# Performance work log

Hardware: AMD Instinct MI355X
Metric: run time of the kernel (lower is better)

Reference implementation:

```python
import jax, jax.numpy as jnp
import numpy as np

D, H = 1024, 2048
N_STEPS = 2
T0, T1 = 0.0, 1.0


def setup_inputs() -> dict:
    key = jax.random.key(0)
    ks = jax.random.split(key, 5)
    s_in = 1.0 / np.sqrt(D)
    s_h = 1.0 / np.sqrt(H)
    return {
        "x0": jax.random.normal(ks[0], (D,), jnp.float32),
        "W1": jax.random.normal(ks[1], (D, H), jnp.float32) * s_in,
        "b1": jnp.zeros((H,), jnp.float32),
        "wt": jax.random.normal(ks[2], (H,), jnp.float32) * 0.1,
        "W2": jax.random.normal(ks[3], (H, H), jnp.float32) * s_h,
        "b2": jnp.zeros((H,), jnp.float32),
        "W3": jax.random.normal(ks[4], (H, D), jnp.float32) * s_h,
        "b3": jnp.zeros((D,), jnp.float32),
    }


def reference(x0, W1, b1, wt, W2, b2, W3, b3):
    dtype = x0.dtype

    def velocity(t, x):
        # 3-layer tanh MLP velocity field with additive time embedding
        h1 = jnp.tanh(x @ W1 + b1 + t * wt)
        h2 = jnp.tanh(h1 @ W2 + b2)
        return h2 @ W3 + b3

    def vel_and_div(t, x):
        # Mirror of _compute_velocity_and_divergence: linearize + vmap(jvp)
        # over identity to get the full Jacobian, then take its trace.
        v, jvp_fun = jax.linearize(lambda z: velocity(t, z), x)
        cols = jax.vmap(jvp_fun)(jnp.eye(D, dtype=dtype))  # [D, D]
        return v, jnp.trace(cols)

    def aug_dyn(t, x):
        v, div = vel_and_div(t, x)
        return v, -div  # (dx/dt, dlogq/dt)

    # Standard-normal base distribution log_prob at x0
    log2pi = jnp.log(jnp.asarray(2.0 * np.pi, dtype=dtype))
    logq0 = -0.5 * jnp.sum(x0 * x0) - 0.5 * D * log2pi

    dt = jnp.asarray((T1 - T0) / N_STEPS, dtype=dtype)

    def rk4_step(carry, i):
        x, logq = carry
        t = T0 + i * dt
        v1, dl1 = aug_dyn(t, x)
        v2, dl2 = aug_dyn(t + 0.5 * dt, x + 0.5 * dt * v1)
        v3, dl3 = aug_dyn(t + 0.5 * dt, x + 0.5 * dt * v2)
        v4, dl4 = aug_dyn(t + dt, x + dt * v3)
        x_new = x + (dt / 6.0) * (v1 + 2.0 * v2 + 2.0 * v3 + v4)
        logq_new = logq + (dt / 6.0) * (dl1 + 2.0 * dl2 + 2.0 * dl3 + dl4)
        return (x_new, logq_new), None

    (x1, logq1), _ = jax.lax.scan(
        rk4_step, (x0, logq0), jnp.arange(N_STEPS, dtype=dtype)
    )
    # concat [x1 (D,), logq1 ()] -> (D+1,) for a single output array
    return jnp.concatenate([x1, logq1[None]])
```

## Files before the change

kernel.cpp:

```cpp
#include <hip/hip_runtime.h>
#include <math.h>

#define DD 1024
#define HH 2048
#define NCB 256

typedef float f32x4 __attribute__((ext_vector_type(4)));
typedef short short8 __attribute__((ext_vector_type(8)));

__device__ __forceinline__ float b2f(unsigned short u) {
    return __uint_as_float(((unsigned int)u) << 16);
}
__device__ __forceinline__ unsigned short f2b(float f) {
    unsigned int x = __float_as_uint(f);
    unsigned int r = (x + 0x7FFFu + ((x >> 16) & 1u)) >> 16;
    return (unsigned short)r;
}
__device__ __forceinline__ float ald(const float* p) {
    return __hip_atomic_load(p, __ATOMIC_RELAXED, __HIP_MEMORY_SCOPE_AGENT);
}
__device__ __forceinline__ void ast(float* p, float v) {
    __hip_atomic_store(p, v, __ATOMIC_RELAXED, __HIP_MEMORY_SCOPE_AGENT);
}

__global__ __launch_bounds__(256) void k_tr(const float* __restrict__ W1,
                                            const float* __restrict__ W2,
                                            const float* __restrict__ W3,
                                            unsigned short* __restrict__ W1T,
                                            unsigned short* __restrict__ W2T,
                                            unsigned short* __restrict__ W3T,
                                            unsigned short* __restrict__ W3b,
                                            unsigned* __restrict__ sync) {
    __shared__ float tile[64][65];
    const int b = blockIdx.x, t = threadIdx.x;
    if (b == 0) {
        #pragma unroll
        for (int q = 0; q < 18; ++q) {
            int i = t + q * 256;
            if (i < 4368) sync[i] = 0u;
        }
    }
    const float* in; unsigned short* out; int R, C, bx, by;
    bool isW3 = false;
    if (b < 512)       { int bb = b;        in = W1; out = W1T; R = DD; C = HH; bx = bb & 31; by = bb >> 5; }
    else if (b < 1536) { int bb = b - 512;  in = W2; out = W2T; R = HH; C = HH; bx = bb & 31; by = bb >> 5; }
    else               { int bb = b - 1536; in = W3; out = W3T; R = HH; C = DD; bx = bb & 15; by = bb >> 4; isW3 = true; }
    const int c0 = bx * 64, r0 = by * 64;
    const int cc = t & 63, rb = t >> 6;
    #pragma unroll
    for (int p = 0; p < 16; ++p) {
        int rr = p * 4 + rb;
        float v = in[(size_t)(r0 + rr) * C + c0 + cc];
        tile[rr][cc] = v;
        if (isW3) W3b[(size_t)(r0 + rr) * DD + c0 + cc] = f2b(v);
    }
    __syncthreads();
    #pragma unroll
    for (int p = 0; p < 16; ++p) {
        int rr = p * 4 + rb;
        out[(size_t)(c0 + rr) * R + r0 + cc] = f2b(tile[cc][rr]);
    }
}

__global__ __launch_bounds__(256) void k_gemmP(const unsigned short* __restrict__ W1T,
                                               const unsigned short* __restrict__ W3b,
                                               const float* __restrict__ W2,
                                               const float* __restrict__ b3,
                                               const float* __restrict__ x0,
                                               unsigned short* __restrict__ Mb,
                                               unsigned short* __restrict__ Pb,
                                               float* __restrict__ c1,
                                               float* __restrict__ A1g) {
    __shared__ unsigned short At[128][40];
    __shared__ unsigned short Bt[128][40];
    const int b = blockIdx.x, t = threadIdx.x;
    const int m0 = (b & 15) * 128;
    const int k0 = (b >> 4) * 128;
    const int r = t & 127, half = t >> 7;
    const int wv = t >> 6, l = t & 63;
    const int wr = wv >> 1, wc = wv & 1;
    const int fr = l & 15, fg = l >> 4;
    const bool do_aux = ((b >> 4) == 0) && (t < 128);
    float c1acc = 0.f, a1acc = 0.f;

    f32x4 acc[4][4] = {};
    for (int i0 = 0; i0 < DD; i0 += 32) {
        {
            const float4* sa = (const float4*)(W1T + (size_t)(m0 + r) * DD + i0 + half * 16);
            const float4* sb = (const float4*)(W3b + (size_t)(k0 + r) * DD + i0 + half * 16);
            float4 a0 = sa[0], a1 = sa[1];
            float4 b0 = sb[0], b1 = sb[1];
            float4* da = (float4*)&At[r][half * 16];
            float4* db = (float4*)&Bt[r][half * 16];
            da[0] = a0; da[1] = a1;
            db[0] = b0; db[1] = b1;
        }
        __syncthreads();
        if (do_aux) {
            #pragma unroll
            for (int i = 0; i < 32; ++i) {
                float w1v = b2f(At[t][i]);
                c1acc += w1v * b3[i0 + i];
                a1acc += w1v * x0[i0 + i];
            }
        }
        short8 af[4], bf[4];
        #pragma unroll
        for (int a = 0; a < 4; ++a)
            af[a] = *(const short8*)&At[wr * 64 + a * 16 + fr][fg * 8];
        #pragma unroll
        for (int bq = 0; bq < 4; ++bq)
            bf[bq] = *(const short8*)&Bt[wc * 64 + bq * 16 + fr][fg * 8];
        #pragma unroll
        for (int a = 0; a < 4; ++a)
            #pragma unroll
            for (int bq = 0; bq < 4; ++bq)
                acc[a][bq] = __builtin_amdgcn_mfma_f32_16x16x32_bf16(af[a], bf[bq], acc[a][bq], 0, 0, 0);
        __syncthreads();
    }
    if (do_aux) { c1[m0 + t] = c1acc; A1g[m0 + t] = a1acc; }
    #pragma unroll
    for (int a = 0; a < 4; ++a) {
        #pragma unroll
        for (int bq = 0; bq < 4; ++bq) {
            #pragma unroll
            for (int j = 0; j < 4; ++j) {
                int row = m0 + wr * 64 + a * 16 + fg * 4 + j;
                int col = k0 + wc * 64 + bq * 16 + fr;
                size_t idx = (size_t)row * HH + col;
                float m = acc[a][bq][j];
                Mb[idx] = f2b(m);
                Pb[idx] = f2b(m * W2[idx]);
            }
        }
    }
}

__device__ __forceinline__ void gbar(unsigned* sync, int b, unsigned g) {
    __syncthreads();
    if (threadIdx.x < 64) {
        if (threadIdx.x == 0) {
            asm volatile("s_waitcnt vmcnt(0)" ::: "memory");
            __hip_atomic_store(&sync[b << 4], g, __ATOMIC_RELAXED, __HIP_MEMORY_SCOPE_AGENT);
        }
        while (true) {
            bool ok = true;
            #pragma unroll
            for (int k = 0; k < 4; ++k) {
                unsigned f = __hip_atomic_load(&sync[(threadIdx.x + (k << 6)) << 4],
                                               __ATOMIC_RELAXED, __HIP_MEMORY_SCOPE_AGENT);
                ok &= (f >= g);
            }
            if (!__any((int)(!ok))) break;
            __builtin_amdgcn_s_sleep(1);
        }
    }
    __syncthreads();
}

__global__ __launch_bounds__(256, 1) void k_chain(
    const unsigned short* __restrict__ Mb,
    const unsigned short* __restrict__ Pb,
    const unsigned short* __restrict__ W2T,
    const unsigned short* __restrict__ W3T,
    const float* __restrict__ x0,
    const float* __restrict__ b1, const float* __restrict__ wt,
    const float* __restrict__ b2, const float* __restrict__ b3,
    const float* __restrict__ c1, const float* __restrict__ A1g,
    float* __restrict__ h1_g, float* __restrict__ h2_g, float* __restrict__ hacc_g,
    float* __restrict__ out,
    unsigned* __restrict__ sync) {
    __shared__ unsigned short Ms[8][2048];
    __shared__ unsigned short Ps[8][2048];
    __shared__ unsigned short Qs[8][2048];
    __shared__ float vecH[2048];
    __shared__ float vecW[2048];
    __shared__ float wred[4];
    const int t = threadIdx.x, b = blockIdx.x;
    const int wib = t >> 6, lane = t & 63;
    const int gw2 = (b << 3) + (wib << 1);
    const int jx = (b << 2) + wib;
    unsigned g = 0;

    {
        const unsigned short* mp = Mb + (size_t)gw2 * HH;
        const unsigned short* pp = Pb + (size_t)gw2 * HH;
        const unsigned short* qp = W2T + (size_t)gw2 * HH;
        #pragma unroll
        for (int rep = 0; rep < 4; ++rep) {
            const int idx = rep * 512 + lane * 8;
            *(short8*)&Ms[wib * 2][idx]     = *(const short8*)(mp + idx);
            *(short8*)&Ms[wib * 2 + 1][idx] = *(const short8*)(mp + HH + idx);
            *(short8*)&Ps[wib * 2][idx]     = *(const short8*)(pp + idx);
            *(short8*)&Ps[wib * 2 + 1][idx] = *(const short8*)(pp + HH + idx);
            *(short8*)&Qs[wib * 2][idx]     = *(const short8*)(qp + idx);
            *(short8*)&Qs[wib * 2 + 1][idx] = *(const short8*)(qp + HH + idx);
        }
    }

    const float bb1_0 = b1[gw2], bb1_1 = b1[gw2 + 1];
    const float wt_0 = wt[gw2], wt_1 = wt[gw2 + 1];
    const float bb2_0 = b2[gw2], bb2_1 = b2[gw2 + 1];
    const float c1_0 = c1[gw2], c1_1 = c1[gw2 + 1];

    float A1_0 = 0.f, A1_1 = 0.f;
    float u0 = 0.f, u1 = 0.f;
    float hc0 = 0.f, hc1 = 0.f;
    float wdiv = 0.f;

    float logq_r = 0.f;
    if (b == 0 && wib == 0) {
        float ssum = 0.f;
        #pragma unroll
        for (int q = 0; q < 16; ++q) { float xv = x0[lane + (q << 6)]; ssum += xv * xv; }
        #pragma unroll
        for (int o = 1; o < 64; o <<= 1) ssum += __shfl_xor(ssum, o, 64);
        logq_r = -0.5f * ssum - 0.5f * 1024.0f * 1.8378770664093453f;
    }

    for (int s = 0; s < 8; ++s) {
        const int ss = s & 3;
        const float tcur = (s >> 2) * 0.5f + ((ss == 0) ? 0.f : (ss == 3) ? 0.5f : 0.25f);

        if (s == 0) {
            A1_0 = A1g[gw2]; A1_1 = A1g[gw2 + 1];
            float h0 = tanhf(A1_0 + bb1_0 + tcur * wt_0);
            float h1v = tanhf(A1_1 + bb1_1 + tcur * wt_1);
            u0 = 1.f - h0 * h0; u1 = 1.f - h1v * h1v;
            if (lane == 0) { ast(h1_g + gw2, h0); ast(h1_g + gw2 + 1, h1v); }
        } else {
            #pragma unroll
            for (int q = 0; q < 8; ++q) {
                int i = t + (q << 8);
                float h2v = ald(h2_g + i);
                float sv = (ss == 0) ? ald(hacc_g + i) : h2v;
                vecH[i] = sv;
                vecW[i] = 1.f - h2v * h2v;
            }
            __syncthreads();
            float md0 = 0.f, md1 = 0.f, pd0 = 0.f, pd1 = 0.f;
            #pragma unroll
            for (int rep = 0; rep < 4; ++rep) {
                const int idx = rep * 512 + lane * 8;
                float4 hA = *(const float4*)(vecH + idx);
                float4 hB = *(const float4*)(vecH + idx + 4);
                float4 wA = *(const float4*)(vecW + idx);
                float4 wB = *(const float4*)(vecW + idx + 4);
                float hv[8] = {hA.x, hA.y, hA.z, hA.w, hB.x, hB.y, hB.z, hB.w};
                float wv[8] = {wA.x, wA.y, wA.z, wA.w, wB.x, wB.y, wB.z, wB.w};
                short8 m0v = *(const short8*)&Ms[wib * 2][idx];
                short8 m1v = *(const short8*)&Ms[wib * 2 + 1][idx];
                short8 p0v = *(const short8*)&Ps[wib * 2][idx];
                short8 p1v = *(const short8*)&Ps[wib * 2 + 1][idx];
                #pragma unroll
                for (int e = 0; e < 8; ++e) {
                    md0 += b2f((unsigned short)m0v[e]) * hv[e];
                    md1 += b2f((unsigned short)m1v[e]) * hv[e];
                    pd0 += b2f((unsigned short)p0v[e]) * wv[e];
                    pd1 += b2f((unsigned short)p1v[e]) * wv[e];
                }
            }
            #pragma unroll
            for (int o = 1; o < 64; o <<= 1) {
                md0 += __shfl_xor(md0, o, 64); md1 += __shfl_xor(md1, o, 64);
                pd0 += __shfl_xor(pd0, o, 64); pd1 += __shfl_xor(pd1, o, 64);
            }
            const int sp = (s - 1) & 3;
            const float cprev = (sp == 1 || sp == 2) ? (1.f / 6.f) : (1.f / 12.f);
            wdiv += cprev * (u0 * pd0 + u1 * pd1);
            float pre0, pre1;
            if (ss == 0) {
                A1_0 += md0 + 0.5f * c1_0; A1_1 += md1 + 0.5f * c1_1;
                pre0 = A1_0 + bb1_0 + tcur * wt_0; pre1 = A1_1 + bb1_1 + tcur * wt_1;
            } else {
                const float a = (ss == 3) ? 0.5f : 0.25f;
                pre0 = A1_0 + a * (md0 + c1_0) + bb1_0 + tcur * wt_0;
                pre1 = A1_1 + a * (md1 + c1_1) + bb1_1 + tcur * wt_1;
            }
            float h0 = tanhf(pre0), h1v = tanhf(pre1);
            u0 = 1.f - h0 * h0; u1 = 1.f - h1v * h1v;
            if (lane == 0) { ast(h1_g + gw2, h0); ast(h1_g + gw2 + 1, h1v); }
        }
        gbar(sync, b, ++g);

        #pragma unroll
        for (int q = 0; q < 8; ++q) {
            int i = t + (q << 8);
            vecH[i] = ald(h1_g + i);
        }
        __syncthreads();
        {
            float a0 = 0.f, a1 = 0.f;
            #pragma unroll
            for (int rep = 0; rep < 4; ++rep) {
                const int idx = rep * 512 + lane * 8;
                float4 hA = *(const float4*)(vecH + idx);
                float4 hB = *(const float4*)(vecH + idx + 4);
                float hv[8] = {hA.x, hA.y, hA.z, hA.w, hB.x, hB.y, hB.z, hB.w};
                short8 r0 = *(const short8*)&Qs[wib * 2][idx];
                short8 r1 = *(const short8*)&Qs[wib * 2 + 1][idx];
                #pragma unroll
                for (int e = 0; e < 8; ++e) {
                    a0 += b2f((unsigned short)r0[e]) * hv[e];
                    a1 += b2f((unsigned short)r1[e]) * hv[e];
                }
            }
            #pragma unroll
            for (int o = 1; o < 64; o <<= 1) {
                a0 += __shfl_xor(a0, o, 64); a1 += __shfl_xor(a1, o, 64);
            }
            float q0 = tanhf(a0 + bb2_0), q1 = tanhf(a1 + bb2_1);
            const float cs = (ss == 1 || ss == 2) ? (1.f / 6.f) : (1.f / 12.f);
            hc0 += cs * q0; hc1 += cs * q1;
            if (lane == 0) {
                ast(h2_g + gw2, q0); ast(h2_g + gw2 + 1, q1);
                if (ss == 3) { ast(hacc_g + gw2, hc0); ast(hacc_g + gw2 + 1, hc1); }
            }
        }
        gbar(sync, b, ++g);
    }

    {
        #pragma unroll
        for (int q = 0; q < 8; ++q) {
            int i = t + (q << 8);
            float h2v = ald(h2_g + i);
            vecH[i] = ald(hacc_g + i);
            vecW[i] = 1.f - h2v * h2v;
        }
        __syncthreads();
        float pd0 = 0.f, pd1 = 0.f, xo = 0.f;
        const unsigned short* Vr = W3T + (size_t)jx * HH;
        #pragma unroll
        for (int rep = 0; rep < 4; ++rep) {
            const int idx = rep * 512 + lane * 8;
            float4 cA = *(const float4*)(vecH + idx);
            float4 cB = *(const float4*)(vecH + idx + 4);
            float4 wA = *(const float4*)(vecW + idx);
            float4 wB = *(const float4*)(vecW + idx + 4);
            float cv[8] = {cA.x, cA.y, cA.z, cA.w, cB.x, cB.y, cB.z, cB.w};
            float wv[8] = {wA.x, wA.y, wA.z, wA.w, wB.x, wB.y, wB.z, wB.w};
            short8 p0v = *(const short8*)&Ps[wib * 2][idx];
            short8 p1v = *(const short8*)&Ps[wib * 2 + 1][idx];
            short8 vv = *(const short8*)(Vr + idx);
            #pragma unroll
            for (int e = 0; e < 8; ++e) {
                pd0 += b2f((unsigned short)p0v[e]) * wv[e];
                pd1 += b2f((unsigned short)p1v[e]) * wv[e];
                xo  += b2f((unsigned short)vv[e]) * cv[e];
            }
        }
        #pragma unroll
        for (int o = 1; o < 64; o <<= 1) {
            pd0 += __shfl_xor(pd0, o, 64); pd1 += __shfl_xor(pd1, o, 64);
            xo += __shfl_xor(xo, o, 64);
        }
        wdiv += (1.f / 12.f) * (u0 * pd0 + u1 * pd1);
        if (lane == 0) {
            out[jx] = x0[jx] + xo + b3[jx];
            wred[wib] = wdiv;
        }
    }
    __syncthreads();
    if (t == 0) {
        float dsum = wred[0] + wred[1] + wred[2] + wred[3];
        atomicAdd((float*)(sync + 4096 + (b & 15) * 16), dsum);
        asm volatile("s_waitcnt vmcnt(0)" ::: "memory");
        atomicAdd(sync + 4352, 1u);
    }
    if (b == 0 && wib == 0) {
        if (lane == 0) {
            while (__hip_atomic_load(sync + 4352, __ATOMIC_RELAXED, __HIP_MEMORY_SCOPE_AGENT) < NCB)
                __builtin_amdgcn_s_sleep(2);
        }
        float v = 0.f;
        if (lane < 16) {
            unsigned du = __hip_atomic_load(sync + 4096 + lane * 16,
                                            __ATOMIC_RELAXED, __HIP_MEMORY_SCOPE_AGENT);
            v = __uint_as_float(du);
        }
        #pragma unroll
        for (int o = 1; o < 64; o <<= 1) v += __shfl_xor(v, o, 64);
        if (lane == 0) out[DD] = logq_r - v;
    }
}

extern "C" void kernel_launch(void* const* d_in, const int* in_sizes, int n_in,
                              void* d_out, int out_size, void* d_ws, size_t ws_size,
                              hipStream_t stream) {
    const float* x0 = (const float*)d_in[0];
    const float* W1 = (const float*)d_in[1];
    const float* b1 = (const float*)d_in[2];
    const float* wt = (const float*)d_in[3];
    const float* W2 = (const float*)d_in[4];
    const float* b2 = (const float*)d_in[5];
    const float* W3 = (const float*)d_in[6];
    const float* b3 = (const float*)d_in[7];
    float* out = (float*)d_out;

    char* ws = (char*)d_ws;
    const size_t MB = 1024 * 1024;
    unsigned short* Pb  = (unsigned short*)(ws);
    unsigned short* W2T = (unsigned short*)(ws + 8 * MB);
    unsigned short* W3T = (unsigned short*)(ws + 16 * MB);
    unsigned short* Mb  = (unsigned short*)(ws + 20 * MB);
    unsigned short* W1T = (unsigned short*)(ws + 28 * MB);
    unsigned short* W3b = (unsigned short*)(ws + 32 * MB);
    float* fb = (float*)(ws + 36 * MB);
    float* c1      = fb;
    float* A1g     = fb + 2048;
    float* h1_g    = fb + 4096;
    float* h2_g    = fb + 6144;
    float* hacc_g  = fb + 8192;
    unsigned* sync = (unsigned*)(fb + 10240);

    k_tr<<<2048, 256, 0, stream>>>(W1, W2, W3, W1T, W2T, W3T, W3b, sync);
    k_gemmP<<<256, 256, 0, stream>>>(W1T, W3b, W2, b3, x0, Mb, Pb, c1, A1g);
    k_chain<<<NCB, 256, 0, stream>>>(Mb, Pb, W2T, W3T, x0, b1, wt, b2, b3, c1, A1g,
                                     h1_g, h2_g, hacc_g, out, sync);
}
```

Baseline: 164.5 us.

## Split global barrier to overlap shared-memory preloads, halve GEMM tile height

The precompute GEMM now uses 64x128 tiles across 512 blocks instead of 128x128 across 256, giving more parallelism on a GPU with many compute units. In the chain kernel the grid barrier is split into separate arrive and wait halves. The W2T and then the M/P matrix loads into shared memory are issued between arrive and wait, so they overlap with the barrier spin. The first stage (h1 and the h2 matvec at t=0) is peeled out of the loop to make this possible. The cost is more code, and the GEMM tiles get less reuse of the B tile.

```diff
diff --git a/kernel.cpp b/kernel.cpp
--- a/kernel.cpp
+++ b/kernel.cpp
@@ -71,28 +71,27 @@
                                                unsigned short* __restrict__ Pb,
                                                float* __restrict__ c1,
                                                float* __restrict__ A1g) {
-    __shared__ unsigned short At[128][40];
+    __shared__ unsigned short At[64][40];
     __shared__ unsigned short Bt[128][40];
     const int b = blockIdx.x, t = threadIdx.x;
-    const int m0 = (b & 15) * 128;
-    const int k0 = (b >> 4) * 128;
-    const int r = t & 127, half = t >> 7;
+    const int m0 = (b & 31) * 64;
+    const int k0 = (b >> 5) * 128;
     const int wv = t >> 6, l = t & 63;
-    const int wr = wv >> 1, wc = wv & 1;
     const int fr = l & 15, fg = l >> 4;
-    const bool do_aux = ((b >> 4) == 0) && (t < 128);
+    const int ra = t & 63, ha = t >> 6;
+    const int rb2 = t & 127, hb = t >> 7;
+    const bool do_aux = ((b >> 5) == 0) && (t < 64);
     float c1acc = 0.f, a1acc = 0.f;
 
-    f32x4 acc[4][4] = {};
+    f32x4 acc[4][2] = {};
     for (int i0 = 0; i0 < DD; i0 += 32) {
         {
-            const float4* sa = (const float4*)(W1T + (size_t)(m0 + r) * DD + i0 + half * 16);
-            const float4* sb = (const float4*)(W3b + (size_t)(k0 + r) * DD + i0 + half * 16);
-            float4 a0 = sa[0], a1 = sa[1];
+            const float4* sa = (const float4*)(W1T + (size_t)(m0 + ra) * DD + i0 + ha * 8);
+            float4 a0 = sa[0];
+            const float4* sb = (const float4*)(W3b + (size_t)(k0 + rb2) * DD + i0 + hb * 16);
             float4 b0 = sb[0], b1 = sb[1];
-            float4* da = (float4*)&At[r][half * 16];
-            float4* db = (float4*)&Bt[r][half * 16];
-            da[0] = a0; da[1] = a1;
+            *(float4*)&At[ra][ha * 8] = a0;
+            float4* db = (float4*)&Bt[rb2][hb * 16];
             db[0] = b0; db[1] = b1;
         }
         __syncthreads();
@@ -104,17 +103,17 @@
                 a1acc += w1v * x0[i0 + i];
             }
         }
-        short8 af[4], bf[4];
+        short8 af[4], bf[2];
         #pragma unroll
         for (int a = 0; a < 4; ++a)
-            af[a] = *(const short8*)&At[wr * 64 + a * 16 + fr][fg * 8];
-        #pragma unroll
-        for (int bq = 0; bq < 4; ++bq)
-            bf[bq] = *(const short8*)&Bt[wc * 64 + bq * 16 + fr][fg * 8];
+            af[a] = *(const short8*)&At[a * 16 + fr][fg * 8];
+        #pragma unroll
+        for (int bq = 0; bq < 2; ++bq)
+            bf[bq] = *(const short8*)&Bt[wv * 32 + bq * 16 + fr][fg * 8];
         #pragma unroll
         for (int a = 0; a < 4; ++a)
             #pragma unroll
-            for (int bq = 0; bq < 4; ++bq)
+            for (int bq = 0; bq < 2; ++bq)
                 acc[a][bq] = __builtin_amdgcn_mfma_f32_16x16x32_bf16(af[a], bf[bq], acc[a][bq], 0, 0, 0);
         __syncthreads();
     }
@@ -122,11 +121,11 @@
     #pragma unroll
     for (int a = 0; a < 4; ++a) {
         #pragma unroll
-        for (int bq = 0; bq < 4; ++bq) {
+        for (int bq = 0; bq < 2; ++bq) {
             #pragma unroll
             for (int j = 0; j < 4; ++j) {
-                int row = m0 + wr * 64 + a * 16 + fg * 4 + j;
-                int col = k0 + wc * 64 + bq * 16 + fr;
+                int row = m0 + a * 16 + fg * 4 + j;
+                int col = k0 + wv * 32 + bq * 16 + fr;
                 size_t idx = (size_t)row * HH + col;
                 float m = acc[a][bq][j];
                 Mb[idx] = f2b(m);
@@ -136,13 +135,15 @@
     }
 }
 
-__device__ __forceinline__ void gbar(unsigned* sync, int b, unsigned g) {
+__device__ __forceinline__ void garrive(unsigned* sync, int b, unsigned g) {
     __syncthreads();
+    if (threadIdx.x == 0) {
+        asm volatile("s_waitcnt vmcnt(0)" ::: "memory");
+        __hip_atomic_store(&sync[b << 4], g, __ATOMIC_RELAXED, __HIP_MEMORY_SCOPE_AGENT);
+    }
+}
+__device__ __forceinline__ void gwait(unsigned* sync, unsigned g) {
     if (threadIdx.x < 64) {
-        if (threadIdx.x == 0) {
-            asm volatile("s_waitcnt vmcnt(0)" ::: "memory");
-            __hip_atomic_store(&sync[b << 4], g, __ATOMIC_RELAXED, __HIP_MEMORY_SCOPE_AGENT);
-        }
         while (true) {
             bool ok = true;
             #pragma unroll
@@ -156,6 +157,10 @@
         }
     }
     __syncthreads();
+}
+__device__ __forceinline__ void gbar(unsigned* sync, int b, unsigned g) {
+    garrive(sync, b, g);
+    gwait(sync, g);
 }
 
 __global__ __launch_bounds__(256, 1) void k_chain(
@@ -182,21 +187,9 @@
     const int jx = (b << 2) + wib;
     unsigned g = 0;
 
-    {
-        const unsigned short* mp = Mb + (size_t)gw2 * HH;
-        const unsigned short* pp = Pb + (size_t)gw2 * HH;
-        const unsigned short* qp = W2T + (size_t)gw2 * HH;
-        #pragma unroll
-        for (int rep = 0; rep < 4; ++rep) {
-            const int idx = rep * 512 + lane * 8;
-            *(short8*)&Ms[wib * 2][idx]     = *(const short8*)(mp + idx);
-            *(short8*)&Ms[wib * 2 + 1][idx] = *(const short8*)(mp + HH + idx);
-            *(short8*)&Ps[wib * 2][idx]     = *(const short8*)(pp + idx);
-            *(short8*)&Ps[wib * 2 + 1][idx] = *(const short8*)(pp + HH + idx);
-            *(short8*)&Qs[wib * 2][idx]     = *(const short8*)(qp + idx);
-            *(short8*)&Qs[wib * 2 + 1][idx] = *(const short8*)(qp + HH + idx);
-        }
-    }
+    const unsigned short* mp = Mb + (size_t)gw2 * HH;
+    const unsigned short* pp = Pb + (size_t)gw2 * HH;
+    const unsigned short* qp = W2T + (size_t)gw2 * HH;
 
     const float bb1_0 = b1[gw2], bb1_1 = b1[gw2 + 1];
     const float wt_0 = wt[gw2], wt_1 = wt[gw2 + 1];
@@ -218,17 +211,70 @@
         logq_r = -0.5f * ssum - 0.5f * 1024.0f * 1.8378770664093453f;
     }
 
-    for (int s = 0; s < 8; ++s) {
+    {
+        A1_0 = A1g[gw2]; A1_1 = A1g[gw2 + 1];
+        float h0 = tanhf(A1_0 + bb1_0);
+        float h1v = tanhf(A1_1 + bb1_1);
+        u0 = 1.f - h0 * h0; u1 = 1.f - h1v * h1v;
+        if (lane == 0) { ast(h1_g + gw2, h0); ast(h1_g + gw2 + 1, h1v); }
+    }
+    garrive(sync, b, ++g);
+    #pragma unroll
+    for (int rep = 0; rep < 4; ++rep) {
+        const int idx = rep * 512 + lane * 8;
+        *(short8*)&Qs[wib * 2][idx]     = *(const short8*)(qp + idx);
+        *(short8*)&Qs[wib * 2 + 1][idx] = *(const short8*)(qp + HH + idx);
+    }
+    gwait(sync, g);
+
+    #pragma unroll
+    for (int q = 0; q < 8; ++q) {
+        int i = t + (q << 8);
+        vecH[i] = ald(h1_g + i);
+    }
+    __syncthreads();
+    {
+        float a0 = 0.f, a1 = 0.f;
+        #pragma unroll
+        for (int rep = 0; rep < 4; ++rep) {
+            const int idx = rep * 512 + lane * 8;
+            float4 hA = *(const float4*)(vecH + idx);
+            float4 hB = *(const float4*)(vecH + idx + 4);
+            float hv[8] = {hA.x, hA.y, hA.z, hA.w, hB.x, hB.y, hB.z, hB.w};
+            short8 r0 = *(const short8*)&Qs[wib * 2][idx];
+            short8 r1 = *(const short8*)&Qs[wib * 2 + 1][idx];
+            #pragma unroll
+            for (int e = 0; e < 8; ++e) {
+                a0 += b2f((unsigned short)r0[e]) * hv[e];
+                a1 += b2f((unsigned short)r1[e]) * hv[e];
+            }
+        }
+        #pragma unroll
+        for (int o = 1; o < 64; o <<= 1) {
+            a0 += __shfl_xor(a0, o, 64); a1 += __shfl_xor(a1, o, 64);
+        }
+        float q0 = tanhf(a0 + bb2_0), q1 = tanhf(a1 + bb2_1);
+        hc0 += (1.f / 12.f) * q0; hc1 += (1.f / 12.f) * q1;
+        if (lane == 0) {
+            ast(h2_g + gw2, q0); ast(h2_g + gw2 + 1, q1);
+        }
+    }
+    garrive(sync, b, ++g);
+    #pragma unroll
+    for (int rep = 0; rep < 4; ++rep) {
+        const int idx = rep * 512 + lane * 8;
+        *(short8*)&Ms[wib * 2][idx]     = *(const short8*)(mp + idx);
+        *(short8*)&Ms[wib * 2 + 1][idx] = *(const short8*)(mp + HH + idx);
+        *(short8*)&Ps[wib * 2][idx]     = *(const short8*)(pp + idx);
+        *(short8*)&Ps[wib * 2 + 1][idx] = *(const short8*)(pp + HH + idx);
+    }
+    gwait(sync, g);
+
+    for (int s = 1; s < 8; ++s) {
         const int ss = s & 3;
         const float tcur = (s >> 2) * 0.5f + ((ss == 0) ? 0.f : (ss == 3) ? 0.5f : 0.25f);
 
-        if (s == 0) {
-            A1_0 = A1g[gw2]; A1_1 = A1g[gw2 + 1];
-            float h0 = tanhf(A1_0 + bb1_0 + tcur * wt_0);
-            float h1v = tanhf(A1_1 + bb1_1 + tcur * wt_1);
-            u0 = 1.f - h0 * h0; u1 = 1.f - h1v * h1v;
-            if (lane == 0) { ast(h1_g + gw2, h0); ast(h1_g + gw2 + 1, h1v); }
-        } else {
+        {
             #pragma unroll
             for (int q = 0; q < 8; ++q) {
                 int i = t + (q << 8);
@@ -415,7 +461,7 @@
     unsigned* sync = (unsigned*)(fb + 10240);
 
     k_tr<<<2048, 256, 0, stream>>>(W1, W2, W3, W1T, W2T, W3T, W3b, sync);
-    k_gemmP<<<256, 256, 0, stream>>>(W1T, W3b, W2, b3, x0, Mb, Pb, c1, A1g);
+    k_gemmP<<<512, 256, 0, stream>>>(W1T, W3b, W2, b3, x0, Mb, Pb, c1, A1g);
     k_chain<<<NCB, 256, 0, stream>>>(Mb, Pb, W2T, W3T, x0, b1, wt, b2, b3, c1, A1g,
                                      h1_g, h2_g, hacc_g, out, sync);
 }
```

Result: faster. 155.5 us (-5.5%).
